# Kernel tuning notes

Measured on AMD Instinct MI355X. Metric: run time of the kernel, lower is better.

Reference implementation:

```python
import jax, jax.numpy as jnp
import numpy as np

N_SRC = 40000
N_TGT = 40000
N_EDGE = 640000
D = 128
LN_EPS = 1e-5


def layer_norm(x, gamma, beta):
    mu = jnp.mean(x, axis=-1, keepdims=True)
    var = jnp.mean((x - mu) ** 2, axis=-1, keepdims=True)
    return (x - mu) * jax.lax.rsqrt(var + LN_EPS) * gamma + beta


def setup_inputs() -> dict:
    key = jax.random.key(0)
    ks = jax.random.split(key, 10)
    src_feat = jax.random.normal(ks[0], (N_SRC, D), dtype=jnp.float32)
    tgt_feat = jax.random.normal(ks[1], (N_TGT, D), dtype=jnp.float32)
    edge_feat = jax.random.normal(ks[2], (N_EDGE, D), dtype=jnp.float32)
    # torch.nn.Linear weights are [out, in]; y = x @ W.T  (bias=False)
    Ws2e = jax.random.normal(ks[3], (D, D), dtype=jnp.float32) * 0.05
    We2e = jax.random.normal(ks[4], (D, D), dtype=jnp.float32) * 0.05
    We2t = jax.random.normal(ks[5], (D, D), dtype=jnp.float32) * 0.05
    Wt2t = jax.random.normal(ks[6], (D, D), dtype=jnp.float32) * 0.05
    src_idx = jax.random.randint(ks[7], (N_EDGE,), 0, N_SRC, dtype=jnp.int32)
    tgt_idx = jax.random.randint(ks[8], (N_EDGE,), 0, N_TGT, dtype=jnp.int32)
    return {
        "src_feat": src_feat, "tgt_feat": tgt_feat, "edge_feat": edge_feat,
        "Ws2e": Ws2e, "We2e": We2e, "We2t": We2t, "Wt2t": Wt2t,
        "gamma1": jnp.ones((D,), jnp.float32), "beta1": jnp.zeros((D,), jnp.float32),
        "gamma2": jnp.ones((D,), jnp.float32), "beta2": jnp.zeros((D,), jnp.float32),
        "src_idx": src_idx, "tgt_idx": tgt_idx,
    }


def reference(src_feat, tgt_feat, edge_feat, Ws2e, We2e, We2t, Wt2t,
              gamma1, beta1, gamma2, beta2, src_idx, tgt_idx):
    # apply_edges(fn.u_add_v): per-edge gather-add of endpoint node features
    node_to_edge = src_feat[src_idx] + tgt_feat[tgt_idx]          # [E, D]
    # edge update: SiLU + LayerNorm over sum of two linears
    add_feat = layer_norm(
        jax.nn.silu(node_to_edge @ Ws2e.T + edge_feat @ We2e.T), gamma1, beta1)
    edge_out = edge_feat + add_feat                               # residual on edges
    # update_all(copy_e, mean): scatter-mean of add_feat onto target nodes
    sums = jax.ops.segment_sum(add_feat, tgt_idx, num_segments=N_TGT)
    counts = jax.ops.segment_sum(jnp.ones((add_feat.shape[0],), add_feat.dtype),
                                 tgt_idx, num_segments=N_TGT)
    agg = sums / jnp.maximum(counts, 1.0)[:, None]                # [N_TGT, D]
    # target node update: SiLU + LayerNorm over sum of two linears, residual
    add_t = layer_norm(jax.nn.silu(agg @ We2t.T + tgt_feat @ Wt2t.T), gamma2, beta2)
    tgt_out = tgt_feat + add_t
    return edge_out, tgt_out
```

## Files before the change

kernel.cpp:

```cpp
#include <hip/hip_runtime.h>
#include <hip/hip_bf16.h>
#include <math.h>

#define D 128
#define DPAD 136
#define BM 64

typedef __attribute__((ext_vector_type(8))) short bf16x8;
typedef __attribute__((ext_vector_type(4))) float f32x4;

__device__ __forceinline__ unsigned short f2bf(float f) {
    unsigned int u = __float_as_uint(f);
    unsigned int r = u + 0x7fffu + ((u >> 16) & 1u);
    return (unsigned short)(r >> 16);
}

__device__ __forceinline__ float silu(float x) {
    return x / (1.f + __expf(-x));
}

__global__ void convert_weights(const float* __restrict__ a, const float* __restrict__ b,
                                const float* __restrict__ c, const float* __restrict__ d,
                                unsigned short* __restrict__ o) {
    int i = blockIdx.x * 256 + threadIdx.x;
    const float* p = (i < 16384) ? a : (i < 32768) ? b : (i < 49152) ? c : d;
    o[i] = f2bf(p[i & 16383]);
}

__global__ void count_edges(const int* __restrict__ tgt_idx, float* __restrict__ counts, int n_edge) {
    int i = blockIdx.x * 256 + threadIdx.x;
    if (i < n_edge) atomicAdd(&counts[tgt_idx[i]], 1.0f);
}


__device__ __forceinline__ void stage_B(const unsigned short* __restrict__ Wb,
                                        unsigned short (*Bs)[DPAD], int tid) {
    const int4* src = (const int4*)Wb;
#pragma unroll
    for (int i = 0; i < 8; ++i) {
        int linear = tid + i * 256;
        int row = linear >> 4, c8 = (linear & 15) * 8;
        *(int4*)&Bs[row][c8] = src[linear];
    }
}

__global__ __launch_bounds__(256) void proj_kernel(const float* __restrict__ A,
                                                   const unsigned short* __restrict__ Wb,
                                                   float* __restrict__ O, int M) {
    __shared__ unsigned short As[BM][DPAD];
    __shared__ unsigned short Bs[D][DPAD];
    int tid = threadIdx.x;
    int m0 = blockIdx.x * BM;
    stage_B(Wb, Bs, tid);
#pragma unroll
    for (int i = 0; i < 8; ++i) {
        int linear = tid + i * 256;
        int row = linear >> 5, c4 = (linear & 31) * 4;
        int gr = m0 + row; if (gr >= M) gr = M - 1;
        float4 v = *(const float4*)&A[(size_t)gr * D + c4];
        unsigned int lo = (unsigned int)f2bf(v.x) | ((unsigned int)f2bf(v.y) << 16);
        unsigned int hi = (unsigned int)f2bf(v.z) | ((unsigned int)f2bf(v.w) << 16);
        *(uint2*)&As[row][c4] = make_uint2(lo, hi);
    }
    __syncthreads();

    int wid = tid >> 6, lane = tid & 63, q = lane >> 4, ln = lane & 15;
    f32x4 acc[8];
#pragma unroll
    for (int nt = 0; nt < 8; ++nt) acc[nt] = (f32x4){0.f, 0.f, 0.f, 0.f};
    int arow = wid * 16 + ln;
#pragma unroll
    for (int k0 = 0; k0 < 128; k0 += 32) {
        bf16x8 a = *(const bf16x8*)&As[arow][k0 + q * 8];
#pragma unroll
        for (int nt = 0; nt < 8; ++nt) {
            bf16x8 b = *(const bf16x8*)&Bs[nt * 16 + ln][k0 + q * 8];
            acc[nt] = __builtin_amdgcn_mfma_f32_16x16x32_bf16(a, b, acc[nt], 0, 0, 0);
        }
    }
#pragma unroll
    for (int r = 0; r < 4; ++r) {
        int grow = m0 + wid * 16 + q * 4 + r;
        if (grow < M) {
#pragma unroll
            for (int nt = 0; nt < 8; ++nt)
                O[(size_t)grow * D + nt * 16 + ln] = acc[nt][r];
        }
    }
}

__global__ __launch_bounds__(256) void edge_kernel(const float* __restrict__ edge_feat,
                                                   const unsigned short* __restrict__ We2e_b,
                                                   const float* __restrict__ Sp,
                                                   const float* __restrict__ Tp,
                                                   const int* __restrict__ src_idx,
                                                   const int* __restrict__ tgt_idx,
                                                   const float* __restrict__ gamma1,
                                                   const float* __restrict__ beta1,
                                                   float* __restrict__ edge_out,
                                                   float* __restrict__ sums,
                                                   int n_edge) {
    __shared__ unsigned short As[BM][DPAD];
    __shared__ unsigned short Bs[D][DPAD];
    int tid = threadIdx.x;
    int e0 = blockIdx.x * BM;
    stage_B(We2e_b, Bs, tid);
#pragma unroll
    for (int i = 0; i < 8; ++i) {
        int linear = tid + i * 256;
        int row = linear >> 5, c4 = (linear & 31) * 4;
        int gr = e0 + row; if (gr >= n_edge) gr = n_edge - 1;
        float4 v = *(const float4*)&edge_feat[(size_t)gr * D + c4];
        unsigned int lo = (unsigned int)f2bf(v.x) | ((unsigned int)f2bf(v.y) << 16);
        unsigned int hi = (unsigned int)f2bf(v.z) | ((unsigned int)f2bf(v.w) << 16);
        *(uint2*)&As[row][c4] = make_uint2(lo, hi);
    }
    __syncthreads();

    int wid = tid >> 6, lane = tid & 63, q = lane >> 4, ln = lane & 15;
    f32x4 acc[8];
#pragma unroll
    for (int nt = 0; nt < 8; ++nt) acc[nt] = (f32x4){0.f, 0.f, 0.f, 0.f};
    int arow = wid * 16 + ln;
#pragma unroll
    for (int k0 = 0; k0 < 128; k0 += 32) {
        bf16x8 a = *(const bf16x8*)&As[arow][k0 + q * 8];
#pragma unroll
        for (int nt = 0; nt < 8; ++nt) {
            bf16x8 b = *(const bf16x8*)&Bs[nt * 16 + ln][k0 + q * 8];
            acc[nt] = __builtin_amdgcn_mfma_f32_16x16x32_bf16(a, b, acc[nt], 0, 0, 0);
        }
    }

    float g[8], bt[8];
#pragma unroll
    for (int nt = 0; nt < 8; ++nt) { g[nt] = gamma1[nt * 16 + ln]; bt[nt] = beta1[nt * 16 + ln]; }

#pragma unroll
    for (int r = 0; r < 4; ++r) {
        int e = e0 + wid * 16 + q * 4 + r;
        if (e >= n_edge) continue;
        int s = src_idx[e], t = tgt_idx[e];
        float h[8], sum = 0.f, sumsq = 0.f;
#pragma unroll
        for (int nt = 0; nt < 8; ++nt) {
            int c = nt * 16 + ln;
            float v = acc[nt][r] + Sp[(size_t)s * D + c] + Tp[(size_t)t * D + c];
            v = silu(v);
            h[nt] = v; sum += v; sumsq += v * v;
        }
#pragma unroll
        for (int m = 1; m < 16; m <<= 1) {
            sum += __shfl_xor(sum, m);
            sumsq += __shfl_xor(sumsq, m);
        }
        float mean = sum * (1.f / 128.f);
        float var = sumsq * (1.f / 128.f) - mean * mean;
        float rs = rsqrtf(var + 1e-5f);
#pragma unroll
        for (int nt = 0; nt < 8; ++nt) {
            int c = nt * 16 + ln;
            float a = (h[nt] - mean) * rs * g[nt] + bt[nt];
            edge_out[(size_t)e * D + c] = edge_feat[(size_t)e * D + c] + a;
            atomicAdd(&sums[(size_t)t * D + c], a);
        }
    }
}

__global__ __launch_bounds__(256) void node_kernel(const float* __restrict__ sums,
                                                   const float* __restrict__ counts,
                                                   const unsigned short* __restrict__ We2t_b,
                                                   const float* __restrict__ Ttp,
                                                   const float* __restrict__ tgt_feat,
                                                   const float* __restrict__ gamma2,
                                                   const float* __restrict__ beta2,
                                                   float* __restrict__ tgt_out,
                                                   int n_tgt) {
    __shared__ unsigned short As[BM][DPAD];
    __shared__ unsigned short Bs[D][DPAD];
    int tid = threadIdx.x;
    int m0 = blockIdx.x * BM;
    stage_B(We2t_b, Bs, tid);
#pragma unroll
    for (int i = 0; i < 8; ++i) {
        int linear = tid + i * 256;
        int row = linear >> 5, c4 = (linear & 31) * 4;
        int gr = m0 + row; if (gr >= n_tgt) gr = n_tgt - 1;
        float rcp = 1.f / fmaxf(counts[gr], 1.f);
        float4 v = *(const float4*)&sums[(size_t)gr * D + c4];
        unsigned int lo = (unsigned int)f2bf(v.x * rcp) | ((unsigned int)f2bf(v.y * rcp) << 16);
        unsigned int hi = (unsigned int)f2bf(v.z * rcp) | ((unsigned int)f2bf(v.w * rcp) << 16);
        *(uint2*)&As[row][c4] = make_uint2(lo, hi);
    }
    __syncthreads();

    int wid = tid >> 6, lane = tid & 63, q = lane >> 4, ln = lane & 15;
    f32x4 acc[8];
#pragma unroll
    for (int nt = 0; nt < 8; ++nt) acc[nt] = (f32x4){0.f, 0.f, 0.f, 0.f};
    int arow = wid * 16 + ln;
#pragma unroll
    for (int k0 = 0; k0 < 128; k0 += 32) {
        bf16x8 a = *(const bf16x8*)&As[arow][k0 + q * 8];
#pragma unroll
        for (int nt = 0; nt < 8; ++nt) {
            bf16x8 b = *(const bf16x8*)&Bs[nt * 16 + ln][k0 + q * 8];
            acc[nt] = __builtin_amdgcn_mfma_f32_16x16x32_bf16(a, b, acc[nt], 0, 0, 0);
        }
    }

    float g[8], bt[8];
#pragma unroll
    for (int nt = 0; nt < 8; ++nt) { g[nt] = gamma2[nt * 16 + ln]; bt[nt] = beta2[nt * 16 + ln]; }

#pragma unroll
    for (int r = 0; r < 4; ++r) {
        int row = m0 + wid * 16 + q * 4 + r;
        if (row >= n_tgt) continue;
        float h[8], sum = 0.f, sumsq = 0.f;
#pragma unroll
        for (int nt = 0; nt < 8; ++nt) {
            int c = nt * 16 + ln;
            float v = acc[nt][r] + Ttp[(size_t)row * D + c];
            v = silu(v);
            h[nt] = v; sum += v; sumsq += v * v;
        }
#pragma unroll
        for (int m = 1; m < 16; m <<= 1) {
            sum += __shfl_xor(sum, m);
            sumsq += __shfl_xor(sumsq, m);
        }
        float mean = sum * (1.f / 128.f);
        float var = sumsq * (1.f / 128.f) - mean * mean;
        float rs = rsqrtf(var + 1e-5f);
#pragma unroll
        for (int nt = 0; nt < 8; ++nt) {
            int c = nt * 16 + ln;
            float a = (h[nt] - mean) * rs * g[nt] + bt[nt];
            tgt_out[(size_t)row * D + c] = tgt_feat[(size_t)row * D + c] + a;
        }
    }
}

extern "C" void kernel_launch(void* const* d_in, const int* in_sizes, int n_in,
                              void* d_out, int out_size, void* d_ws, size_t ws_size,
                              hipStream_t stream) {
    const float* src_feat  = (const float*)d_in[0];
    const float* tgt_feat  = (const float*)d_in[1];
    const float* edge_feat = (const float*)d_in[2];
    const float* Ws2e = (const float*)d_in[3];
    const float* We2e = (const float*)d_in[4];
    const float* We2t = (const float*)d_in[5];
    const float* Wt2t = (const float*)d_in[6];
    const float* gamma1 = (const float*)d_in[7];
    const float* beta1  = (const float*)d_in[8];
    const float* gamma2 = (const float*)d_in[9];
    const float* beta2  = (const float*)d_in[10];
    const int* src_idx = (const int*)d_in[11];
    const int* tgt_idx = (const int*)d_in[12];

    int n_src  = in_sizes[0] / D;
    int n_tgt  = in_sizes[1] / D;
    int n_edge = in_sizes[2] / D;

    float* edge_out = (float*)d_out;
    float* tgt_out  = (float*)d_out + (size_t)n_edge * D;

    char* ws = (char*)d_ws;
    unsigned short* Wb = (unsigned short*)ws;
    float* Sp     = (float*)(ws + 4 * 16384 * 2);
    float* Tp     = Sp + (size_t)n_src * D;
    float* Ttp    = Tp + (size_t)n_tgt * D;
    float* sums   = Ttp + (size_t)n_tgt * D;
    float* counts = sums + (size_t)n_tgt * D;

    hipMemsetAsync(sums, 0, ((size_t)n_tgt * D + n_tgt) * sizeof(float), stream);

    convert_weights<<<256, 256, 0, stream>>>(Ws2e, We2e, We2t, Wt2t, Wb);
    count_edges<<<(n_edge + 255) / 256, 256, 0, stream>>>(tgt_idx, counts, n_edge);

    proj_kernel<<<(n_src + BM - 1) / BM, 256, 0, stream>>>(src_feat, Wb,             Sp,  n_src);
    proj_kernel<<<(n_tgt + BM - 1) / BM, 256, 0, stream>>>(tgt_feat, Wb,             Tp,  n_tgt);
    proj_kernel<<<(n_tgt + BM - 1) / BM, 256, 0, stream>>>(tgt_feat, Wb + 3 * 16384, Ttp, n_tgt);

    edge_kernel<<<(n_edge + BM - 1) / BM, 256, 0, stream>>>(
        edge_feat, Wb + 16384, Sp, Tp, src_idx, tgt_idx, gamma1, beta1,
        edge_out, sums, n_edge);

    node_kernel<<<(n_tgt + BM - 1) / BM, 256, 0, stream>>>(
        sums, counts, Wb + 2 * 16384, Ttp, tgt_feat, gamma2, beta2,
        tgt_out, n_tgt);
}
```

Baseline: 884.9 us.

## Sort edges by target via counting sort and pre-reduce runs before atomics

Builds a CSR-style permutation of edges grouped by target node (count, scan, fill) and processes edges in that order in the edge kernel. Within each block, consecutive rows with the same target are summed in shared memory so that only one set of atomics per run goes to global sums. This is meant to cut contention and the volume of global float atomics, at the cost of several extra small kernels and gathered, non-contiguous edge_feat reads and edge_out writes. Tp reads for the same target also become more cache-friendly.

```diff
diff --git a/kernel.cpp b/kernel.cpp
--- a/kernel.cpp
+++ b/kernel.cpp
@@ -27,9 +27,61 @@
     o[i] = f2bf(p[i & 16383]);
 }
 
-__global__ void count_edges(const int* __restrict__ tgt_idx, float* __restrict__ counts, int n_edge) {
+__global__ void count_edges(const int* __restrict__ tgt_idx, int* __restrict__ cnt, int n_edge) {
     int i = blockIdx.x * 256 + threadIdx.x;
-    if (i < n_edge) atomicAdd(&counts[tgt_idx[i]], 1.0f);
+    if (i < n_edge) atomicAdd(&cnt[tgt_idx[i]], 1);
+}
+
+
+__global__ void scan_chunks(const int* __restrict__ cnt, int* __restrict__ chunk_sum, int n) {
+    int i = blockIdx.x * 256 + threadIdx.x;
+    int v = (i < n) ? cnt[i] : 0;
+#pragma unroll
+    for (int m = 1; m < 64; m <<= 1) v += __shfl_xor(v, m);
+    __shared__ int ws[4];
+    if ((threadIdx.x & 63) == 0) ws[threadIdx.x >> 6] = v;
+    __syncthreads();
+    if (threadIdx.x == 0) chunk_sum[blockIdx.x] = ws[0] + ws[1] + ws[2] + ws[3];
+}
+
+__global__ void scan_offsets(int* __restrict__ chunk_sum, int nc) {
+    int tid = threadIdx.x;
+    int v = (tid < nc) ? chunk_sum[tid] : 0;
+    int lane = tid & 63, w = tid >> 6;
+    int s = v;
+#pragma unroll
+    for (int m = 1; m < 64; m <<= 1) { int t = __shfl_up(s, m); if (lane >= m) s += t; }
+    __shared__ int wsum[4];
+    if (lane == 63) wsum[w] = s;
+    __syncthreads();
+    int base = 0;
+    for (int k = 0; k < w; ++k) base += wsum[k];
+    if (tid < nc) chunk_sum[tid] = base + s - v;
+}
+
+__global__ void scan_final(const int* __restrict__ cnt, const int* __restrict__ chunk_off,
+                           int* __restrict__ cursor, int n) {
+    int tid = threadIdx.x, i = blockIdx.x * 256 + tid;
+    int v = (i < n) ? cnt[i] : 0;
+    int lane = tid & 63, w = tid >> 6;
+    int s = v;
+#pragma unroll
+    for (int m = 1; m < 64; m <<= 1) { int t = __shfl_up(s, m); if (lane >= m) s += t; }
+    __shared__ int wsum[4];
+    if (lane == 63) wsum[w] = s;
+    __syncthreads();
+    int base = chunk_off[blockIdx.x];
+    for (int k = 0; k < w; ++k) base += wsum[k];
+    if (i < n) cursor[i] = base + s - v;
+}
+
+__global__ void fill_edges(const int* __restrict__ tgt_idx, int* __restrict__ cursor,
+                           int* __restrict__ edge_ids, int n_edge) {
+    int i = blockIdx.x * 256 + threadIdx.x;
+    if (i < n_edge) {
+        int p = atomicAdd(&cursor[tgt_idx[i]], 1);
+        edge_ids[p] = i;
+    }
 }
 
 
@@ -95,25 +147,38 @@
                                                    const float* __restrict__ Tp,
                                                    const int* __restrict__ src_idx,
                                                    const int* __restrict__ tgt_idx,
+                                                   const int* __restrict__ edge_ids,
                                                    const float* __restrict__ gamma1,
                                                    const float* __restrict__ beta1,
                                                    float* __restrict__ edge_out,
                                                    float* __restrict__ sums,
                                                    int n_edge) {
-    __shared__ unsigned short As[BM][DPAD];
-    __shared__ unsigned short Bs[D][DPAD];
+    __shared__ union {
+        struct { unsigned short As[BM][DPAD]; unsigned short Bs[D][DPAD]; } ab;
+        float Fs[BM][D];
+    } sm;
+    __shared__ int eid_s[BM];
+    __shared__ int trow_s[BM];
+
     int tid = threadIdx.x;
     int e0 = blockIdx.x * BM;
-    stage_B(We2e_b, Bs, tid);
+
+    if (tid < BM) {
+        int ge = e0 + tid;
+        eid_s[tid] = edge_ids[ge < n_edge ? ge : n_edge - 1];
+    }
+    stage_B(We2e_b, sm.ab.Bs, tid);
+    __syncthreads();
+
 #pragma unroll
     for (int i = 0; i < 8; ++i) {
         int linear = tid + i * 256;
         int row = linear >> 5, c4 = (linear & 31) * 4;
-        int gr = e0 + row; if (gr >= n_edge) gr = n_edge - 1;
-        float4 v = *(const float4*)&edge_feat[(size_t)gr * D + c4];
+        int e = eid_s[row];
+        float4 v = *(const float4*)&edge_feat[(size_t)e * D + c4];
         unsigned int lo = (unsigned int)f2bf(v.x) | ((unsigned int)f2bf(v.y) << 16);
         unsigned int hi = (unsigned int)f2bf(v.z) | ((unsigned int)f2bf(v.w) << 16);
-        *(uint2*)&As[row][c4] = make_uint2(lo, hi);
+        *(uint2*)&sm.ab.As[row][c4] = make_uint2(lo, hi);
     }
     __syncthreads();
 
@@ -124,10 +189,10 @@
     int arow = wid * 16 + ln;
 #pragma unroll
     for (int k0 = 0; k0 < 128; k0 += 32) {
-        bf16x8 a = *(const bf16x8*)&As[arow][k0 + q * 8];
-#pragma unroll
-        for (int nt = 0; nt < 8; ++nt) {
-            bf16x8 b = *(const bf16x8*)&Bs[nt * 16 + ln][k0 + q * 8];
+        bf16x8 a = *(const bf16x8*)&sm.ab.As[arow][k0 + q * 8];
+#pragma unroll
+        for (int nt = 0; nt < 8; ++nt) {
+            bf16x8 b = *(const bf16x8*)&sm.ab.Bs[nt * 16 + ln][k0 + q * 8];
             acc[nt] = __builtin_amdgcn_mfma_f32_16x16x32_bf16(a, b, acc[nt], 0, 0, 0);
         }
     }
@@ -136,11 +201,15 @@
 #pragma unroll
     for (int nt = 0; nt < 8; ++nt) { g[nt] = gamma1[nt * 16 + ln]; bt[nt] = beta1[nt * 16 + ln]; }
 
+    __syncthreads();
+
 #pragma unroll
     for (int r = 0; r < 4; ++r) {
-        int e = e0 + wid * 16 + q * 4 + r;
-        if (e >= n_edge) continue;
+        int row = wid * 16 + q * 4 + r;
+        bool valid = (e0 + row) < n_edge;
+        int e = eid_s[row];
         int s = src_idx[e], t = tgt_idx[e];
+        if (ln == 0) trow_s[row] = valid ? t : -1;
         float h[8], sum = 0.f, sumsq = 0.f;
 #pragma unroll
         for (int nt = 0; nt < 8; ++nt) {
@@ -161,14 +230,44 @@
         for (int nt = 0; nt < 8; ++nt) {
             int c = nt * 16 + ln;
             float a = (h[nt] - mean) * rs * g[nt] + bt[nt];
-            edge_out[(size_t)e * D + c] = edge_feat[(size_t)e * D + c] + a;
-            atomicAdd(&sums[(size_t)t * D + c], a);
+            sm.Fs[row][c] = a;
+            if (valid)
+                edge_out[(size_t)e * D + c] = edge_feat[(size_t)e * D + c] + a;
+        }
+    }
+    __syncthreads();
+
+    {
+        int row = tid >> 2, part = tid & 3;
+        int t = trow_s[row];
+        bool head = (t >= 0) && (row == 0 || trow_s[row - 1] != t);
+        if (head) {
+            int L = 1;
+            while (row + L < BM && trow_s[row + L] == t) ++L;
+            f32x4 a4[8];
+#pragma unroll
+            for (int k = 0; k < 8; ++k) a4[k] = (f32x4){0.f, 0.f, 0.f, 0.f};
+            for (int j = 0; j < L; ++j) {
+                const float* fp = &sm.Fs[row + j][part * 32];
+#pragma unroll
+                for (int k = 0; k < 8; ++k) {
+                    f32x4 v = *(const f32x4*)&fp[k * 4];
+                    a4[k] += v;
+                }
+            }
+            float* sp = &sums[(size_t)t * D + part * 32];
+#pragma unroll
+            for (int k = 0; k < 8; ++k) {
+#pragma unroll
+                for (int j = 0; j < 4; ++j)
+                    unsafeAtomicAdd(&sp[k * 4 + j], a4[k][j]);
+            }
         }
     }
 }
 
 __global__ __launch_bounds__(256) void node_kernel(const float* __restrict__ sums,
-                                                   const float* __restrict__ counts,
+                                                   const int* __restrict__ cnt,
                                                    const unsigned short* __restrict__ We2t_b,
                                                    const float* __restrict__ Ttp,
                                                    const float* __restrict__ tgt_feat,
@@ -186,7 +285,7 @@
         int linear = tid + i * 256;
         int row = linear >> 5, c4 = (linear & 31) * 4;
         int gr = m0 + row; if (gr >= n_tgt) gr = n_tgt - 1;
-        float rcp = 1.f / fmaxf(counts[gr], 1.f);
+        float rcp = 1.f / fmaxf((float)cnt[gr], 1.f);
         float4 v = *(const float4*)&sums[(size_t)gr * D + c4];
         unsigned int lo = (unsigned int)f2bf(v.x * rcp) | ((unsigned int)f2bf(v.y * rcp) << 16);
         unsigned int hi = (unsigned int)f2bf(v.z * rcp) | ((unsigned int)f2bf(v.w * rcp) << 16);
@@ -272,22 +371,30 @@
     float* Tp     = Sp + (size_t)n_src * D;
     float* Ttp    = Tp + (size_t)n_tgt * D;
     float* sums   = Ttp + (size_t)n_tgt * D;
-    float* counts = sums + (size_t)n_tgt * D;
+    int*   cnt    = (int*)(sums + (size_t)n_tgt * D);
+    int*   cursor = cnt + n_tgt;
+    int*   chunk  = cursor + n_tgt;
+    int nc = (n_tgt + 255) / 256;
+    int*   edge_ids = chunk + ((nc + 63) & ~63);
 
     hipMemsetAsync(sums, 0, ((size_t)n_tgt * D + n_tgt) * sizeof(float), stream);
 
     convert_weights<<<256, 256, 0, stream>>>(Ws2e, We2e, We2t, Wt2t, Wb);
-    count_edges<<<(n_edge + 255) / 256, 256, 0, stream>>>(tgt_idx, counts, n_edge);
+    count_edges<<<(n_edge + 255) / 256, 256, 0, stream>>>(tgt_idx, cnt, n_edge);
+    scan_chunks<<<nc, 256, 0, stream>>>(cnt, chunk, n_tgt);
+    scan_offsets<<<1, 256, 0, stream>>>(chunk, nc);
+    scan_final<<<nc, 256, 0, stream>>>(cnt, chunk, cursor, n_tgt);
+    fill_edges<<<(n_edge + 255) / 256, 256, 0, stream>>>(tgt_idx, cursor, edge_ids, n_edge);
 
     proj_kernel<<<(n_src + BM - 1) / BM, 256, 0, stream>>>(src_feat, Wb,             Sp,  n_src);
     proj_kernel<<<(n_tgt + BM - 1) / BM, 256, 0, stream>>>(tgt_feat, Wb,             Tp,  n_tgt);
     proj_kernel<<<(n_tgt + BM - 1) / BM, 256, 0, stream>>>(tgt_feat, Wb + 3 * 16384, Ttp, n_tgt);
 
     edge_kernel<<<(n_edge + BM - 1) / BM, 256, 0, stream>>>(
-        edge_feat, Wb + 16384, Sp, Tp, src_idx, tgt_idx, gamma1, beta1,
+        edge_feat, Wb + 16384, Sp, Tp, src_idx, tgt_idx, edge_ids, gamma1, beta1,
         edge_out, sums, n_edge);
 
     node_kernel<<<(n_tgt + BM - 1) / BM, 256, 0, stream>>>(
-        sums, counts, Wb + 2 * 16384, Ttp, tgt_feat, gamma2, beta2,
+        sums, cnt, Wb + 2 * 16384, Ttp, tgt_feat, gamma2, beta2,
         tgt_out, n_tgt);
 }
```

After: 1.166 ms. +31.7%, slower.
